# Optimization experiments

Measured on AMD Instinct MI355X. Metric: run time of the kernel, lower is better.

Reference implementation:

```python
import jax, jax.numpy as jnp
import numpy as np

D_MODEL = 2048
N_HEADS = 16
N_KV_HEADS = 4
HEAD_DIM = 128
ROPE_THETA = 10000.0


def _rope_cos_sin(T, hd, theta):
    # [T, hd//2]
    inv_freq = 1.0 / (theta ** (jnp.arange(0, hd, 2, dtype=jnp.float32) / hd))
    ang = jnp.arange(T, dtype=jnp.float32)[:, None] * inv_freq[None, :]
    return jnp.cos(ang), jnp.sin(ang)


def _apply_rope(x, cos, sin):
    # x: [B, H, T, hd]; rotate-half (Llama-style) RoPE
    hd = x.shape[-1]
    x1, x2 = x[..., : hd // 2], x[..., hd // 2 :]
    c = cos[None, None, :, :]
    s = sin[None, None, :, :]
    return jnp.concatenate([x1 * c - x2 * s, x2 * c + x1 * s], axis=-1)


def setup_inputs() -> dict:
    key = jax.random.key(0)
    ks = jax.random.split(key, 5)
    B, T = 2, 2048
    x = jax.random.normal(ks[0], (B, T, D_MODEL), dtype=jnp.float32)
    sq = 1.0 / np.sqrt(D_MODEL)
    Wq = jax.random.normal(ks[1], (D_MODEL, N_HEADS * HEAD_DIM), dtype=jnp.float32) * sq
    Wk = jax.random.normal(ks[2], (D_MODEL, N_KV_HEADS * HEAD_DIM), dtype=jnp.float32) * sq
    Wv = jax.random.normal(ks[3], (D_MODEL, N_KV_HEADS * HEAD_DIM), dtype=jnp.float32) * sq
    Wo = jax.random.normal(ks[4], (N_HEADS * HEAD_DIM, D_MODEL), dtype=jnp.float32) * sq
    return {"x": x, "Wq": Wq, "Wk": Wk, "Wv": Wv, "Wo": Wo}


def reference(x, Wq, Wk, Wv, Wo):
    B, T, _ = x.shape
    H, KV, hd = N_HEADS, N_KV_HEADS, HEAD_DIM
    n_rep = H // KV

    q = (x @ Wq).reshape(B, T, H, hd).transpose(0, 2, 1, 3)    # [B,H,T,hd]
    k = (x @ Wk).reshape(B, T, KV, hd).transpose(0, 2, 1, 3)   # [B,KV,T,hd]
    v = (x @ Wv).reshape(B, T, KV, hd).transpose(0, 2, 1, 3)

    cos, sin = _rope_cos_sin(T, hd, ROPE_THETA)
    q = _apply_rope(q, cos, sin)
    k = _apply_rope(k, cos, sin)

    # repeat KV heads for GQA: [B,KV,T,hd] -> [B,H,T,hd]
    k = jnp.repeat(k, n_rep, axis=1)
    v = jnp.repeat(v, n_rep, axis=1)

    scale = 1.0 / jnp.sqrt(jnp.float32(hd))
    scores = jnp.einsum("bhqd,bhkd->bhqk", q, k) * scale       # [B,H,T,T]
    causal = jnp.tril(jnp.ones((T, T), dtype=bool))
    scores = jnp.where(causal[None, None, :, :], scores, -jnp.inf)
    attn = jax.nn.softmax(scores, axis=-1)
    out = jnp.einsum("bhqk,bhkd->bhqd", attn, v)               # [B,H,T,hd]
    out = out.transpose(0, 2, 1, 3).reshape(B, T, H * hd)
    return out @ Wo
```

## Files before the change

### kernel.cpp

```cpp
#include <hip/hip_runtime.h>
#include <stdint.h>

#define T_SEQ 2048
#define DM    2048
#define NH    16
#define NKV   4
#define HD    128
#define MROWS 4096
#define NQKV  3072

typedef unsigned short u16;
typedef __bf16 bf16x8 __attribute__((ext_vector_type(8)));
typedef float  f32x4  __attribute__((ext_vector_type(4)));

__device__ __forceinline__ u16 f2b(float f) {
  union { float f; unsigned u; } v; v.f = f;
  return (u16)((v.u + 0x7fffu + ((v.u >> 16) & 1u)) >> 16);
}
__device__ __forceinline__ float b2f(u16 u) {
  union { unsigned u; float f; } v; v.u = ((unsigned)u) << 16;
  return v.f;
}
__device__ __forceinline__ void gl_lds16(const u16* g, u16* l) {
  __builtin_amdgcn_global_load_lds(
      (__attribute__((address_space(1))) void*)g,
      (__attribute__((address_space(3))) void*)l, 16, 0, 0);
}
__device__ __forceinline__ void storev(float* p, float v) { *p = v; }
__device__ __forceinline__ void storev(u16* p, float v)   { *p = f2b(v); }

__global__ __launch_bounds__(256) void k_cvt_x(const float* __restrict__ x,
                                               u16* __restrict__ o, int n) {
  int i = (blockIdx.x * 256 + threadIdx.x) * 4;
  if (i >= n) return;
  float4 v = *(const float4*)(x + i);
  ushort4 r;
  r.x = f2b(v.x); r.y = f2b(v.y); r.z = f2b(v.z); r.w = f2b(v.w);
  *(ushort4*)(o + i) = r;
}

__global__ __launch_bounds__(256) void k_tw4(const float* __restrict__ Wq,
                                             const float* __restrict__ Wk,
                                             const float* __restrict__ Wv,
                                             const float* __restrict__ Wo,
                                             u16* __restrict__ WT,
                                             u16* __restrict__ Wot) {
  __shared__ float tl[32][33];
  int z = blockIdx.z;
  const float* in; u16* out; int Nd, xt;
  if (z < 64)      { in = Wq; out = WT;               Nd = 2048; xt = z; }
  else if (z < 80) { in = Wk; out = WT + 2048 * 2048; Nd = 512;  xt = z - 64; }
  else if (z < 96) { in = Wv; out = WT + 2560 * 2048; Nd = 512;  xt = z - 80; }
  else             { in = Wo; out = Wot;              Nd = 2048; xt = z - 96; }
  int n0 = xt * 32, k0 = blockIdx.y * 32;
  int tx = threadIdx.x, ty = threadIdx.y;
#pragma unroll
  for (int i = 0; i < 32; i += 8)
    tl[ty + i][tx] = in[(long)(k0 + ty + i) * Nd + n0 + tx];
  __syncthreads();
#pragma unroll
  for (int i = 0; i < 32; i += 8)
    out[(long)(n0 + ty + i) * 2048 + k0 + tx] = f2b(tl[tx][ty + i]);
}

template <typename OutT>
__global__ __launch_bounds__(256) void k_gemm(const u16* __restrict__ A,
                                              const u16* __restrict__ Bt,
                                              OutT* __restrict__ C,
                                              int M, int N, int K) {
  __shared__ __align__(16) u16 As[128 * 32];
  __shared__ __align__(16) u16 Bs[128 * 32];
  const int tid = threadIdx.x;
  const int wv = tid >> 6, lane = tid & 63;
  const int quad = lane >> 4, ln = lane & 15;
  const int wm = wv & 1, wn = wv >> 1;
  const int rchnk = quad ^ ((ln >> 1) & 3);
  const long m0 = (long)blockIdx.x * 128;
  const long n0 = (long)blockIdx.y * 128;
  f32x4 acc[4][4] = {};
  for (int k0 = 0; k0 < K; k0 += 32) {
#pragma unroll
    for (int r = 0; r < 2; ++r) {
      int c = r * 256 + tid;
      int gc = (c & 3) ^ ((c >> 3) & 3);
      gl_lds16(A  + (m0 + (c >> 2)) * K + k0 + gc * 8, &As[(r * 256 + wv * 64) * 8]);
      gl_lds16(Bt + (n0 + (c >> 2)) * K + k0 + gc * 8, &Bs[(r * 256 + wv * 64) * 8]);
    }
    __syncthreads();
    bf16x8 af[4], bg[4];
#pragma unroll
    for (int i = 0; i < 4; ++i)
      af[i] = *(const bf16x8*)&As[(wm * 64 + i * 16 + ln) * 32 + rchnk * 8];
#pragma unroll
    for (int j = 0; j < 4; ++j)
      bg[j] = *(const bf16x8*)&Bs[(wn * 64 + j * 16 + ln) * 32 + rchnk * 8];
#pragma unroll
    for (int i = 0; i < 4; ++i)
#pragma unroll
      for (int j = 0; j < 4; ++j)
        acc[i][j] = __builtin_amdgcn_mfma_f32_16x16x32_bf16(af[i], bg[j], acc[i][j], 0, 0, 0);
    __syncthreads();
  }
#pragma unroll
  for (int i = 0; i < 4; ++i) {
    long row = m0 + wm * 64 + i * 16 + quad * 4;
#pragma unroll
    for (int j = 0; j < 4; ++j) {
      long col = n0 + wn * 64 + j * 16 + ln;
#pragma unroll
      for (int r = 0; r < 4; ++r)
        storev(&C[(row + r) * N + col], acc[i][j][r]);
    }
  }
}

__global__ __launch_bounds__(256) void k_rope2(const u16* __restrict__ C,
                                               u16* __restrict__ Qo,
                                               u16* __restrict__ Ko) {
  int idx = blockIdx.x * 256 + threadIdx.x;
  int d = idx & 63;
  int t = (idx >> 6) & (T_SEQ - 1);
  int g = idx >> 17;
  int b = (g >= 20) ? 1 : 0;
  int hh = g - b * 20;
  int isQ = hh < 16;
  int head = isQ ? hh : (hh - 16);
  int coloff = isQ ? 0 : 2048;
  float qscale = isQ ? 0.12751745f : 1.0f;
  u16* o = isQ ? Qo : Ko;
  int nh = isQ ? NH : NKV;
  long inb = (long)(b * T_SEQ + t) * NQKV + coloff + head * HD + d;
  float q1 = b2f(C[inb]);
  float q2 = b2f(C[inb + 64]);
  float inv = __expf(-0.14391156f * (float)d);
  float sn, cs;
  __sincosf((float)t * inv, &sn, &cs);
  long ob = (((long)b * nh + head) * T_SEQ + t) * HD + d;
  o[ob]      = f2b((q1 * cs - q2 * sn) * qscale);
  o[ob + 64] = f2b((q2 * cs + q1 * sn) * qscale);
}

__global__ __launch_bounds__(256) void k_vt(const u16* __restrict__ C,
                                            u16* __restrict__ Vt) {
  __shared__ u16 tl[32][33];
  int bkv = blockIdx.z;
  int t0 = blockIdx.x * 32, d0 = blockIdx.y * 32;
  int tx = threadIdx.x, ty = threadIdx.y;
  int b = bkv >> 2, kv = bkv & 3;
#pragma unroll
  for (int i = 0; i < 32; i += 8)
    tl[ty + i][tx] = C[(long)(b * T_SEQ + t0 + ty + i) * NQKV + 2560 + kv * HD + d0 + tx];
  __syncthreads();
#pragma unroll
  for (int i = 0; i < 32; i += 8)
    Vt[((long)bkv * HD + d0 + ty + i) * T_SEQ + t0 + tx] = tl[tx][ty + i];
}

template <bool DIAG>
__device__ __forceinline__ void p_emit(f32x4 (&S)[4], u16* __restrict__ Pb,
                                       int quad, int ln, int mrow) {
#pragma unroll
  for (int nt = 0; nt < 4; ++nt)
#pragma unroll
    for (int r = 0; r < 4; ++r) {
      float v = S[nt][r];
      if (DIAG) v = (nt * 16 + ln <= mrow + r) ? v : -1e30f;
      float pv = exp2f(v - 8.0f);
      int row = quad * 4 + r;
      int chnk = (nt * 2 + (ln >> 3)) ^ (row & 7);
      *(__bf16*)&Pb[row * 64 + chnk * 8 + (ln & 7)] = (__bf16)pv;
    }
}

__global__ __launch_bounds__(256, 2) void k_attn(const u16* __restrict__ Q,
                                                 const u16* __restrict__ Kg,
                                                 const u16* __restrict__ Vt,
                                                 u16* __restrict__ Og) {
  __shared__ __align__(16) u16 Ks[64 * 128];
  __shared__ __align__(16) u16 Vs[128 * 64];
  __shared__ __align__(16) u16 Ps[4][2][16 * 64];
  const int tid = threadIdx.x;
  const int wv = tid >> 6, lane = tid & 63;
  const int quad = lane >> 4, ln = lane & 15;
  const int bh = blockIdx.y;
  const int b = bh >> 4, h = bh & 15;
  const int kvh = h >> 2;
  const int p = blockIdx.x;
  const int thi = 31 - p, tlo = p;
  const int qhi = thi * 64 + wv * 16;
  const int qlo = tlo * 64 + wv * 16;

  bf16x8 qfh[4], qfl[4];
  {
    const u16* qp = Q + ((long)bh * T_SEQ + qhi + ln) * HD + quad * 8;
#pragma unroll
    for (int s = 0; s < 4; ++s) qfh[s] = *(const bf16x8*)(qp + s * 32);
    qp = Q + ((long)bh * T_SEQ + qlo + ln) * HD + quad * 8;
#pragma unroll
    for (int s = 0; s < 4; ++s) qfl[s] = *(const bf16x8*)(qp + s * 32);
  }
  bf16x8 onesb;
#pragma unroll
  for (int i = 0; i < 8; ++i) onesb[i] = (__bf16)1.0f;

  f32x4 lh = {0.f, 0.f, 0.f, 0.f}, ll = {0.f, 0.f, 0.f, 0.f};
  f32x4 oh[8] = {}, ol[8] = {};

  const u16* Kb = Kg + (long)(b * NKV + kvh) * T_SEQ * HD;
  const u16* Vb = Vt + (long)(b * NKV + kvh) * HD * T_SEQ;

  for (int kt = 0; kt <= thi; ++kt) {
    const int k0 = kt * 64;
#pragma unroll
    for (int r = 0; r < 4; ++r) {
      int s = r * 256 + tid;
      gl_lds16(Kb + (long)(k0 + (s >> 4)) * HD + (((s & 15) ^ ((s >> 4) & 15)) << 3),
               &Ks[(r * 256 + wv * 64) * 8]);
      gl_lds16(Vb + (long)(s >> 3) * T_SEQ + k0 + (((s & 7) ^ ((s >> 3) & 7)) << 3),
               &Vs[(r * 256 + wv * 64) * 8]);
    }
    __syncthreads();
    const bool lo_act = (kt <= tlo);
    f32x4 Sh[4], Sl[4];
#pragma unroll
    for (int nt = 0; nt < 4; ++nt) {
      bf16x8 kb[4];
      const u16* kp = &Ks[(nt * 16 + ln) * 128];
#pragma unroll
      for (int ss = 0; ss < 4; ++ss)
        kb[ss] = *(const bf16x8*)(kp + (((quad + 4 * ss) ^ ln) << 3));
      f32x4 s = {0.f, 0.f, 0.f, 0.f};
#pragma unroll
      for (int ss = 0; ss < 4; ++ss)
        s = __builtin_amdgcn_mfma_f32_16x16x32_bf16(qfh[ss], kb[ss], s, 0, 0, 0);
      Sh[nt] = s;
      if (lo_act) {
        f32x4 t = {0.f, 0.f, 0.f, 0.f};
#pragma unroll
        for (int ss = 0; ss < 4; ++ss)
          t = __builtin_amdgcn_mfma_f32_16x16x32_bf16(qfl[ss], kb[ss], t, 0, 0, 0);
        Sl[nt] = t;
      }
    }
    if (kt == thi) p_emit<true>(Sh, &Ps[wv][0][0], quad, ln, wv * 16 + quad * 4);
    else           p_emit<false>(Sh, &Ps[wv][0][0], quad, ln, 0);
    if (lo_act) {
      if (kt == tlo) p_emit<true>(Sl, &Ps[wv][1][0], quad, ln, wv * 16 + quad * 4);
      else           p_emit<false>(Sl, &Ps[wv][1][0], quad, ln, 0);
    }
    asm volatile("s_waitcnt lgkmcnt(0)" ::: "memory");
    bf16x8 pfh[2], pfl[2];
#pragma unroll
    for (int ss = 0; ss < 2; ++ss)
      pfh[ss] = *(const bf16x8*)&Ps[wv][0][ln * 64 + (((ss * 4 + quad) ^ (ln & 7)) << 3)];
    if (lo_act) {
#pragma unroll
      for (int ss = 0; ss < 2; ++ss)
        pfl[ss] = *(const bf16x8*)&Ps[wv][1][ln * 64 + (((ss * 4 + quad) ^ (ln & 7)) << 3)];
    }
    lh = __builtin_amdgcn_mfma_f32_16x16x32_bf16(pfh[0], onesb, lh, 0, 0, 0);
    lh = __builtin_amdgcn_mfma_f32_16x16x32_bf16(pfh[1], onesb, lh, 0, 0, 0);
    if (lo_act) {
      ll = __builtin_amdgcn_mfma_f32_16x16x32_bf16(pfl[0], onesb, ll, 0, 0, 0);
      ll = __builtin_amdgcn_mfma_f32_16x16x32_bf16(pfl[1], onesb, ll, 0, 0, 0);
    }
#pragma unroll
    for (int dt = 0; dt < 8; ++dt) {
      bf16x8 vb[2];
      const u16* vp = &Vs[(dt * 16 + ln) * 64];
#pragma unroll
      for (int ss = 0; ss < 2; ++ss)
        vb[ss] = *(const bf16x8*)(vp + (((quad + 4 * ss) ^ (ln & 7)) << 3));
#pragma unroll
      for (int ss = 0; ss < 2; ++ss)
        oh[dt] = __builtin_amdgcn_mfma_f32_16x16x32_bf16(pfh[ss], vb[ss], oh[dt], 0, 0, 0);
      if (lo_act) {
#pragma unroll
        for (int ss = 0; ss < 2; ++ss)
          ol[dt] = __builtin_amdgcn_mfma_f32_16x16x32_bf16(pfl[ss], vb[ss], ol[dt], 0, 0, 0);
      }
    }
    __syncthreads();
  }
  float rh[4], rl[4];
#pragma unroll
  for (int r = 0; r < 4; ++r) { rh[r] = 1.f / lh[r]; rl[r] = 1.f / ll[r]; }
#pragma unroll
  for (int dt = 0; dt < 8; ++dt)
#pragma unroll
    for (int r = 0; r < 4; ++r) {
      long rowh = (long)b * T_SEQ + qhi + quad * 4 + r;
      long rowl = (long)b * T_SEQ + qlo + quad * 4 + r;
      Og[rowh * (NH * HD) + h * HD + dt * 16 + ln] = f2b(oh[dt][r] * rh[r]);
      Og[rowl * (NH * HD) + h * HD + dt * 16 + ln] = f2b(ol[dt][r] * rl[r]);
    }
}

extern "C" void kernel_launch(void* const* d_in, const int* in_sizes, int n_in,
                              void* d_out, int out_size, void* d_ws, size_t ws_size,
                              hipStream_t stream) {
  const float* x  = (const float*)d_in[0];
  const float* Wq = (const float*)d_in[1];
  const float* Wk = (const float*)d_in[2];
  const float* Wv = (const float*)d_in[3];
  const float* Wo = (const float*)d_in[4];
  float* out = (float*)d_out;
  char* ws = (char*)d_ws;
  u16* WT  = (u16*)(ws + 0);
  u16* Wot = (u16*)(ws + 12582912);
  u16* Cq  = (u16*)(ws + 20971520);
  u16* Xb  = (u16*)(ws + 46137344);
  u16* Kb  = (u16*)(ws + 62914560);
  u16* Vtb = (u16*)(ws + 67108864);
  u16* Qb = Xb;
  u16* attn = Cq;

  k_cvt_x<<<8192, 256, 0, stream>>>(x, Xb, MROWS * DM);
  k_tw4<<<dim3(1, 64, 160), dim3(32, 8), 0, stream>>>(Wq, Wk, Wv, Wo, WT, Wot);

  k_gemm<u16><<<dim3(32, 24), 256, 0, stream>>>(Xb, WT, Cq, MROWS, NQKV, DM);

  k_rope2<<<20480, 256, 0, stream>>>(Cq, Qb, Kb);
  k_vt<<<dim3(64, 4, 8), dim3(32, 8), 0, stream>>>(Cq, Vtb);

  k_attn<<<dim3(16, 32), 256, 0, stream>>>(Qb, Kb, Vtb, attn);

  k_gemm<float><<<dim3(32, 16), 256, 0, stream>>>(attn, Wot, out, MROWS, DM, 2048);
}
```

Baseline: 314.3 us.

## Replace GEMM with 256-row double-buffered 8-wave pipelined MFMA kernel

The single-stage 128x128 GEMM is replaced by an 8-wave kernel with 256xBN tiles and K-step 64. Global-to-LDS loads for A (one tile ahead) and B (two tiles ahead) are interleaved with four MFMA quadrant phases, using explicit waitcnt, barriers and setprio. The goal is to hide memory latency behind compute and to get more reuse from each LDS tile. The trade-off is fewer blocks: 192 for the QKV GEMM, which underfills a 256-CU device. It also raises register and LDS pressure, and the hand-written synchronisation carries correctness risk.

```diff
diff --git a/kernel.cpp b/kernel.cpp
--- a/kernel.cpp
+++ b/kernel.cpp
@@ -63,50 +63,110 @@
     out[(long)(n0 + ty + i) * 2048 + k0 + tx] = f2b(tl[tx][ty + i]);
 }
 
-template <typename OutT>
-__global__ __launch_bounds__(256) void k_gemm(const u16* __restrict__ A,
-                                              const u16* __restrict__ Bt,
-                                              OutT* __restrict__ C,
-                                              int M, int N, int K) {
-  __shared__ __align__(16) u16 As[128 * 32];
-  __shared__ __align__(16) u16 Bs[128 * 32];
+template <int BN, typename OutT>
+__global__ __launch_bounds__(512, 2) void k_gemm8(const u16* __restrict__ A,
+                                                  const u16* __restrict__ Bt,
+                                                  OutT* __restrict__ C,
+                                                  int M, int N, int K) {
+  constexpr int NJ = BN / 128;
+  constexpr int BH = NJ;
+  __shared__ __align__(16) u16 As[2][256 * 64];
+  __shared__ __align__(16) u16 Bs[2][BN * 64];
   const int tid = threadIdx.x;
   const int wv = tid >> 6, lane = tid & 63;
-  const int quad = lane >> 4, ln = lane & 15;
+  const int quad = lane >> 4, ln = lane & 15, ln7 = lane & 7 & 7;
   const int wm = wv & 1, wn = wv >> 1;
-  const int rchnk = quad ^ ((ln >> 1) & 3);
-  const long m0 = (long)blockIdx.x * 128;
-  const long n0 = (long)blockIdx.y * 128;
-  f32x4 acc[4][4] = {};
-  for (int k0 = 0; k0 < K; k0 += 32) {
-#pragma unroll
-    for (int r = 0; r < 2; ++r) {
-      int c = r * 256 + tid;
-      int gc = (c & 3) ^ ((c >> 3) & 3);
-      gl_lds16(A  + (m0 + (c >> 2)) * K + k0 + gc * 8, &As[(r * 256 + wv * 64) * 8]);
-      gl_lds16(Bt + (n0 + (c >> 2)) * K + k0 + gc * 8, &Bs[(r * 256 + wv * 64) * 8]);
-    }
-    __syncthreads();
-    bf16x8 af[4], bg[4];
-#pragma unroll
-    for (int i = 0; i < 4; ++i)
-      af[i] = *(const bf16x8*)&As[(wm * 64 + i * 16 + ln) * 32 + rchnk * 8];
-#pragma unroll
-    for (int j = 0; j < 4; ++j)
-      bg[j] = *(const bf16x8*)&Bs[(wn * 64 + j * 16 + ln) * 32 + rchnk * 8];
-#pragma unroll
-    for (int i = 0; i < 4; ++i)
-#pragma unroll
-      for (int j = 0; j < 4; ++j)
-        acc[i][j] = __builtin_amdgcn_mfma_f32_16x16x32_bf16(af[i], bg[j], acc[i][j], 0, 0, 0);
-    __syncthreads();
+  const long m0 = (long)blockIdx.x * 256;
+  const long n0 = (long)blockIdx.y * BN;
+  const int so = wv << 1;
+  const int lr8 = lane >> 3;
+  const int gch = (lane & 7) ^ lr8;
+
+  f32x4 acc[8][2 * NJ] = {};
+  bf16x8 Af[4][2], Bf[2 * NJ][2];
+
+  auto stage = [&](const u16* __restrict__ G, long grow0, long kcol, u16* lds) {
+#pragma unroll
+    for (int o = 0; o < 2; ++o) {
+      int lr = (so + o) * 8;
+      gl_lds16(G + (grow0 + lr + lr8) * (long)K + kcol + gch * 8, lds + lr * 64);
+    }
+  };
+
+#define READ_A(MH)                                                            \
+  _Pragma("unroll") for (int i = 0; i < 4; ++i)                               \
+      _Pragma("unroll") for (int s = 0; s < 2; ++s)                           \
+          Af[i][s] = *(const bf16x8*)&asc[((MH)*64 + i * 16 + ln) * 64 +      \
+                                          (((s * 4 + quad) ^ (ln & 7)) << 3)];
+#define READ_B(NHq)                                                           \
+  _Pragma("unroll") for (int jj = 0; jj < NJ; ++jj)                           \
+      _Pragma("unroll") for (int s = 0; s < 2; ++s)                           \
+          Bf[(NHq)*NJ + jj][s] =                                              \
+              *(const bf16x8*)&bsc[(((NHq)*NJ + jj) * 16 + ln) * 64 +         \
+                                   (((s * 4 + quad) ^ (ln & 7)) << 3)];
+#define MMA_Q(MH, NHq)                                                        \
+  _Pragma("unroll") for (int i = 0; i < 4; ++i)                               \
+      _Pragma("unroll") for (int jj = 0; jj < NJ; ++jj) {                     \
+        acc[(MH)*4 + i][(NHq)*NJ + jj] =                                      \
+            __builtin_amdgcn_mfma_f32_16x16x32_bf16(                          \
+                Af[i][0], Bf[(NHq)*NJ + jj][0],                               \
+                acc[(MH)*4 + i][(NHq)*NJ + jj], 0, 0, 0);                     \
+        acc[(MH)*4 + i][(NHq)*NJ + jj] =                                      \
+            __builtin_amdgcn_mfma_f32_16x16x32_bf16(                          \
+                Af[i][1], Bf[(NHq)*NJ + jj][1],                               \
+                acc[(MH)*4 + i][(NHq)*NJ + jj], 0, 0, 0);                     \
+      }
+#define PH_MID()                                                              \
+  __builtin_amdgcn_s_barrier();                                               \
+  asm volatile("s_waitcnt lgkmcnt(0)" ::: "memory");                          \
+  __builtin_amdgcn_s_setprio(1)
+#define PH_END()                                                              \
+  __builtin_amdgcn_s_setprio(0);                                              \
+  __builtin_amdgcn_s_barrier()
+
+  const int NT = K >> 6;
+  stage(Bt, n0, 0, Bs[0]);
+  if (BH == 2) stage(Bt, n0 + 128, 0, Bs[0] + 128 * 64);
+  stage(A, m0, 0, As[0]);
+  stage(A, m0 + 128, 0, As[0] + 128 * 64);
+  stage(Bt, n0, 64, Bs[1]);
+  if (BH == 2) stage(Bt, n0 + 128, 64, Bs[1] + 128 * 64);
+  asm volatile("s_waitcnt vmcnt(%0)" ::"i"(2 * BH) : "memory");
+  __builtin_amdgcn_s_barrier();
+
+  for (int t = 0; t < NT; ++t) {
+    const int par = t & 1;
+    const u16* asc = As[par] + wm * (128 * 64);
+    const u16* bsc = Bs[par] + wn * (32 * NJ * 64);
+    u16* an = As[par ^ 1];
+    u16* bp = Bs[par];
+    const bool pa = (t + 1 < NT), pb = (t + 2 < NT);
+    if (pa) stage(A, m0, (long)(t + 1) * 64, an);
+    READ_A(0); READ_B(0);
+    PH_MID(); MMA_Q(0, 0); PH_END();
+    if (pa) stage(A, m0 + 128, (long)(t + 1) * 64, an + 128 * 64);
+    READ_B(1);
+    PH_MID(); MMA_Q(0, 1); PH_END();
+    if (pb) stage(Bt, n0, (long)(t + 2) * 64, bp);
+    READ_A(1);
+    PH_MID(); MMA_Q(1, 1); PH_END();
+    if (BH == 2 && pb) stage(Bt, n0 + 128, (long)(t + 2) * 64, bp + 128 * 64);
+    if (pb) asm volatile("s_waitcnt vmcnt(%0)" ::"i"(2 * BH) : "memory");
+    else    asm volatile("s_waitcnt vmcnt(0)" ::: "memory");
+    PH_MID(); MMA_Q(1, 0); PH_END();
   }
-#pragma unroll
-  for (int i = 0; i < 4; ++i) {
-    long row = m0 + wm * 64 + i * 16 + quad * 4;
-#pragma unroll
-    for (int j = 0; j < 4; ++j) {
-      long col = n0 + wn * 64 + j * 16 + ln;
+#undef READ_A
+#undef READ_B
+#undef MMA_Q
+#undef PH_MID
+#undef PH_END
+  (void)ln7;
+#pragma unroll
+  for (int i = 0; i < 8; ++i) {
+    long row = m0 + wm * 128 + i * 16 + quad * 4;
+#pragma unroll
+    for (int j = 0; j < 2 * NJ; ++j) {
+      long col = n0 + wn * (32 * NJ) + j * 16 + ln;
 #pragma unroll
       for (int r = 0; r < 4; ++r)
         storev(&C[(row + r) * N + col], acc[i][j][r]);
@@ -318,12 +378,12 @@
   k_cvt_x<<<8192, 256, 0, stream>>>(x, Xb, MROWS * DM);
   k_tw4<<<dim3(1, 64, 160), dim3(32, 8), 0, stream>>>(Wq, Wk, Wv, Wo, WT, Wot);
 
-  k_gemm<u16><<<dim3(32, 24), 256, 0, stream>>>(Xb, WT, Cq, MROWS, NQKV, DM);
+  k_gemm8<256, u16><<<dim3(16, 12), 512, 0, stream>>>(Xb, WT, Cq, MROWS, NQKV, DM);
 
   k_rope2<<<20480, 256, 0, stream>>>(Cq, Qb, Kb);
   k_vt<<<dim3(64, 4, 8), dim3(32, 8), 0, stream>>>(Cq, Vtb);
 
   k_attn<<<dim3(16, 32), 256, 0, stream>>>(Qb, Kb, Vtb, attn);
 
-  k_gemm<float><<<dim3(32, 16), 256, 0, stream>>>(attn, Wot, out, MROWS, DM, 2048);
-}
+  k_gemm8<128, float><<<dim3(16, 16), 512, 0, stream>>>(attn, Wot, out, MROWS, DM, 2048);
+}
```

Result: slower. 333.0 us (+5.9%).
